# Optimization experiments

Measured on AMD Instinct MI355X. Metric: run time of the kernel, lower is better.

Reference implementation:

```python
import jax, jax.numpy as jnp
import numpy as np

N_NODES = 512
STATE_DIM = 16
MESSAGE_DIM = 32
HID_MSG = 64
HID_RO = 64
N_STEPS = 5


def setup_inputs() -> dict:
    key = jax.random.key(0)
    ks = jax.random.split(key, 16)
    s, m, hm, hr = STATE_DIM, MESSAGE_DIM, HID_MSG, HID_RO
    gru_in = s + m
    k_gru = 1.0 / np.sqrt(s)
    inp = {
        'J': jax.random.normal(ks[0], (N_NODES, N_NODES), jnp.float32),
        'b': jax.random.normal(ks[1], (N_NODES,), jnp.float32),
        # message MLP (torch init: weight ~ N(0, 0.1), bias = 0)
        'W1': 0.1 * jax.random.normal(ks[2], (hm, 2 * s + 3), jnp.float32),
        'b1': jnp.zeros((hm,), jnp.float32),
        'W2': 0.1 * jax.random.normal(ks[3], (hm, hm), jnp.float32),
        'b2': jnp.zeros((hm,), jnp.float32),
        'W3': 0.1 * jax.random.normal(ks[4], (m, hm), jnp.float32),
        'b3': jnp.zeros((m,), jnp.float32),
        # GRUCell params (torch default: U(-1/sqrt(hidden), 1/sqrt(hidden)))
        'W_ih': jax.random.uniform(ks[5], (3 * s, gru_in), jnp.float32, -k_gru, k_gru),
        'b_ih': jnp.zeros((3 * s,), jnp.float32),
        'W_hh': jax.random.uniform(ks[6], (3 * s, s), jnp.float32, -k_gru, k_gru),
        'b_hh': jnp.zeros((3 * s,), jnp.float32),
        # readout MLP
        'Wr1': 0.1 * jax.random.normal(ks[7], (hr, s), jnp.float32),
        'br1': jnp.zeros((hr,), jnp.float32),
        'Wr2': 0.1 * jax.random.normal(ks[8], (hr, hr), jnp.float32),
        'br2': jnp.zeros((hr,), jnp.float32),
        'Wr3': 0.1 * jax.random.normal(ks[9], (2, hr), jnp.float32),
        'br3': jnp.zeros((2,), jnp.float32),
    }
    return inp


def _gru_cell(x, h, W_ih, b_ih, W_hh, b_hh):
    s = h.shape[-1]
    gi = x @ W_ih.T + b_ih  # (n, 3s)
    gh = h @ W_hh.T + b_hh  # (n, 3s)
    ir, iz, in_ = gi[:, :s], gi[:, s:2 * s], gi[:, 2 * s:]
    hr, hz, hn = gh[:, :s], gh[:, s:2 * s], gh[:, 2 * s:]
    r = jax.nn.sigmoid(ir + hr)
    z = jax.nn.sigmoid(iz + hz)
    n = jnp.tanh(in_ + r * hn)
    return (1.0 - z) * n + z * h


def reference(J, b, W1, b1, W2, b2, W3, b3, W_ih, b_ih, W_hh, b_hh,
              Wr1, br1, Wr2, br2, Wr3, br3):
    n = J.shape[0]
    s = W_hh.shape[1]
    # Split first message-MLP layer by input blocks [h_i | h_j | J_ij | b_i | b_j]
    # so we never materialize the (n, n, 2s+3) feature tensor.
    W1_hi = W1[:, :s]            # (hm, s)
    W1_hj = W1[:, s:2 * s]       # (hm, s)
    w_J = W1[:, 2 * s]           # (hm,)
    w_bi = W1[:, 2 * s + 1]      # (hm,)
    w_bj = W1[:, 2 * s + 2]      # (hm,)
    # static per-pair part of layer-1 preactivation: (n, n, hm)
    static1 = (J[:, :, None] * w_J
               + b[:, None, None] * w_bi
               + b[None, :, None] * w_bj
               + b1)

    h0 = jnp.zeros((n, s), jnp.float32)

    def step(h, _):
        pre = (h @ W1_hi.T)[:, None, :] + (h @ W1_hj.T)[None, :, :] + static1
        x = jax.nn.relu(pre)                      # (n, n, hm)
        x = jax.nn.relu(x @ W2.T + b2)            # (n, n, hm)
        msg = x @ W3.T + b3                       # (n, n, m)
        m_j = msg.sum(axis=0)                     # sum over i -> (n, m)
        gru_in = jnp.concatenate([h, m_j], axis=1)
        h_new = _gru_cell(gru_in, h, W_ih, b_ih, W_hh, b_hh)
        return h_new, None

    h, _ = jax.lax.scan(step, h0, None, length=N_STEPS)

    y = jax.nn.relu(h @ Wr1.T + br1)
    y = jax.nn.relu(y @ Wr2.T + br2)
    y = jax.nn.sigmoid(y @ Wr3.T + br3)           # (n, 2)
    y = y / jnp.sum(y, axis=1, keepdims=True)
    return y
```

## Files before the change

kernel.cpp:

```cpp
#include <hip/hip_runtime.h>
#include <hip/hip_bf16.h>

#define NN 512
#define SDIM 16
#define MDIM 32
#define HM 64
#define NSTEPS 5

typedef __attribute__((ext_vector_type(8))) short short8;
typedef __attribute__((ext_vector_type(4))) float floatx4;

static __device__ __forceinline__ unsigned short f2bf(float f) {
    union { float f; unsigned u; } x; x.f = f;
    unsigned r = x.u + 0x7fffu + ((x.u >> 16) & 1u);
    return (unsigned short)(r >> 16);
}

__global__ void init_kernel(const float* __restrict__ J, const float* __restrict__ b,
                            const float* __restrict__ W1, const float* __restrict__ b1,
                            const float* __restrict__ W2,
                            float* __restrict__ Jt, float* __restrict__ aG, float* __restrict__ cG,
                            float* __restrict__ h0, float* __restrict__ wJ,
                            unsigned short* __restrict__ W2bf)
{
    int bx = blockIdx.x, tid = threadIdx.x;
    if (bx < 64) {
        __shared__ float tile[64][65];
        int ti = bx >> 3, tj = bx & 7;
        for (int p = 0; p < 16; ++p) {
            int e = p*256 + tid; int r = e >> 6, c = e & 63;
            tile[r][c] = J[(ti*64 + r)*512 + tj*64 + c];
        }
        __syncthreads();
        for (int p = 0; p < 16; ++p) {
            int e = p*256 + tid; int r = e >> 6, c = e & 63;
            Jt[(tj*64 + r)*512 + ti*64 + c] = tile[c][r];
        }
    } else if (bx < 96) {
        int gid = (bx - 64)*256 + tid;
        for (int p = 0; p < 4; ++p) {
            int idx = p*8192 + gid;
            int i = idx >> 6, o = idx & 63;
            aG[idx] = b[i] * W1[o*35 + 33];
        }
    } else if (bx < 128) {
        int gid = (bx - 96)*256 + tid;
        for (int p = 0; p < 4; ++p) {
            int idx = p*8192 + gid;
            int i = idx >> 6, o = idx & 63;
            cG[idx] = b[i] * W1[o*35 + 34] + b1[o];
        }
    } else if (bx == 128) {
        for (int p = 0; p < 16; ++p) {
            int flat = p*256 + tid;
            int jj = flat & 7;
            int lane = (flat >> 3) & 63;
            int tk = flat >> 9;
            int nt = tk >> 1, ks = tk & 1;
            int n = nt*16 + (lane & 15);
            int k = ks*32 + (lane >> 4)*8 + jj;
            W2bf[flat] = f2bf(W2[n*64 + k]);
        }
        if (tid < 64) wJ[tid] = W1[tid*35 + 32];
    } else {
        for (int p = 0; p < 32; ++p) h0[p*256 + tid] = 0.f;
    }
}

__global__ __launch_bounds__(256) void edge_kernel(
    const float* __restrict__ Jt,
    const float* __restrict__ aIn, const float* __restrict__ cIn, const float* __restrict__ hIn,
    float* __restrict__ aOut, float* __restrict__ cOut, float* __restrict__ hOut,
    const unsigned short* __restrict__ W2bf, const float* __restrict__ wJ,
    const float* __restrict__ b2, const float* __restrict__ W3, const float* __restrict__ b3,
    const float* __restrict__ W_ih, const float* __restrict__ b_ih,
    const float* __restrict__ W_hh, const float* __restrict__ b_hh,
    const float* __restrict__ W1, const float* __restrict__ bvec, const float* __restrict__ b1)
{
    const int j = blockIdx.x;
    const int tid = threadIdx.x;
    const int l = tid & 63, w = tid >> 6;
    const int m = l & 15, q = l >> 4;

    __shared__ float smWave[4][64];
    __shared__ float smMacc[64];
    __shared__ float smMsg[32];
    __shared__ float smGi[48], smGh[48];
    __shared__ float smH[16];

    const floatx4* c4 = (const floatx4*)cIn;
    const floatx4* w4 = (const floatx4*)wJ;
    floatx4 cva = c4[j*16 + q*2],     cvb = c4[j*16 + q*2 + 1];
    floatx4 cvc = c4[j*16 + 8 + q*2], cvd = c4[j*16 + 8 + q*2 + 1];
    floatx4 wva = w4[q*2], wvb = w4[q*2+1], wvc = w4[8+q*2], wvd = w4[8+q*2+1];

    short8 bf[4][2];
    {
        const short8* wb = (const short8*)W2bf;
        #pragma unroll
        for (int nt = 0; nt < 4; ++nt)
            #pragma unroll
            for (int ks = 0; ks < 2; ++ks)
                bf[nt][ks] = wb[(nt*2 + ks)*64 + l];
    }
    float b2n[4];
    #pragma unroll
    for (int nt = 0; nt < 4; ++nt) b2n[nt] = b2[nt*16 + m];

    floatx4 acc[4];
    #pragma unroll
    for (int nt = 0; nt < 4; ++nt) acc[nt] = (floatx4){0.f,0.f,0.f,0.f};

    const floatx4* a4 = (const floatx4*)aIn;

    for (int c8 = 0; c8 < 8; ++c8) {
        int i = w*128 + c8*16 + m;
        float Jij = Jt[j*512 + i];
        floatx4 av0 = a4[i*16 + q*2],     av1 = a4[i*16 + q*2 + 1];
        floatx4 av2 = a4[i*16 + 8 + q*2], av3 = a4[i*16 + 8 + q*2 + 1];
        floatx4 x0, x1, x2, x3;
        #pragma unroll
        for (int e = 0; e < 4; ++e) {
            x0[e] = fmaxf(fmaf(Jij, wva[e], av0[e]) + cva[e], 0.f);
            x1[e] = fmaxf(fmaf(Jij, wvb[e], av1[e]) + cvb[e], 0.f);
            x2[e] = fmaxf(fmaf(Jij, wvc[e], av2[e]) + cvc[e], 0.f);
            x3[e] = fmaxf(fmaf(Jij, wvd[e], av3[e]) + cvd[e], 0.f);
        }
        short8 fa0, fa1;
        #pragma unroll
        for (int e = 0; e < 4; ++e) {
            fa0[e]   = (short)f2bf(x0[e]);
            fa0[e+4] = (short)f2bf(x1[e]);
            fa1[e]   = (short)f2bf(x2[e]);
            fa1[e+4] = (short)f2bf(x3[e]);
        }
        #pragma unroll
        for (int nt = 0; nt < 4; ++nt) {
            floatx4 d = {0.f,0.f,0.f,0.f};
            d = __builtin_amdgcn_mfma_f32_16x16x32_bf16(fa0, bf[nt][0], d, 0, 0, 0);
            d = __builtin_amdgcn_mfma_f32_16x16x32_bf16(fa1, bf[nt][1], d, 0, 0, 0);
            #pragma unroll
            for (int r = 0; r < 4; ++r)
                acc[nt][r] += fmaxf(d[r] + b2n[nt], 0.f);
        }
    }

    #pragma unroll
    for (int nt = 0; nt < 4; ++nt) {
        float v = acc[nt][0] + acc[nt][1] + acc[nt][2] + acc[nt][3];
        v += __shfl_xor(v, 16);
        v += __shfl_xor(v, 32);
        if (l < 16) smWave[w][nt*16 + l] = v;
    }
    __syncthreads();
    if (tid < 64) smMacc[tid] = smWave[0][tid] + smWave[1][tid] + smWave[2][tid] + smWave[3][tid];
    __syncthreads();
    if (tid < 32) {
        float s = 512.f * b3[tid];
        for (int k = 0; k < 64; ++k) s += W3[tid*64 + k] * smMacc[k];
        smMsg[tid] = s;
    }
    __syncthreads();
    if (tid < 48) {
        float gi = b_ih[tid];
        for (int c = 0; c < 16; ++c) gi += W_ih[tid*48 + c] * hIn[j*16 + c];
        for (int c = 0; c < 32; ++c) gi += W_ih[tid*48 + 16 + c] * smMsg[c];
        float gh = b_hh[tid];
        for (int s = 0; s < 16; ++s) gh += W_hh[tid*16 + s] * hIn[j*16 + s];
        smGi[tid] = gi; smGh[tid] = gh;
    }
    __syncthreads();
    if (tid < 16) {
        float r = 1.f / (1.f + __expf(-(smGi[tid] + smGh[tid])));
        float z = 1.f / (1.f + __expf(-(smGi[16+tid] + smGh[16+tid])));
        float n = tanhf(smGi[32+tid] + r * smGh[32+tid]);
        float hn = (1.f - z)*n + z*hIn[j*16 + tid];
        hOut[j*16 + tid] = hn;
        smH[tid] = hn;
    }
    __syncthreads();
    if (tid < 64) {
        int o = tid;
        float da = 0.f, dc = 0.f;
        for (int s = 0; s < 16; ++s) {
            da += W1[o*35 + s]      * smH[s];
            dc += W1[o*35 + 16 + s] * smH[s];
        }
        aOut[j*64 + o] = da + bvec[j]*W1[o*35+33];
        cOut[j*64 + o] = dc + bvec[j]*W1[o*35+34] + b1[o];
    }
}

__global__ void readout_kernel(const float* __restrict__ h,
    const float* __restrict__ Wr1, const float* __restrict__ br1,
    const float* __restrict__ Wr2, const float* __restrict__ br2,
    const float* __restrict__ Wr3, const float* __restrict__ br3,
    float* __restrict__ out)
{
    int tid = threadIdx.x; int l = tid & 63, w = tid >> 6;
    int node = blockIdx.x*4 + w;
    __shared__ float sm[4][64];
    float y1 = br1[l];
    for (int s = 0; s < 16; ++s) y1 += Wr1[l*16 + s] * h[node*16 + s];
    y1 = fmaxf(y1, 0.f);
    sm[w][l] = y1;
    __syncthreads();
    float y2 = br2[l];
    for (int k = 0; k < 64; ++k) y2 += Wr2[l*64 + k] * sm[w][k];
    y2 = fmaxf(y2, 0.f);
    __syncthreads();
    sm[w][l] = y2;
    __syncthreads();
    if (l == 0) {
        float s0 = br3[0], s1 = br3[1];
        for (int k = 0; k < 64; ++k) { s0 += Wr3[k]*sm[w][k]; s1 += Wr3[64+k]*sm[w][k]; }
        float e0 = 1.f/(1.f + __expf(-s0));
        float e1 = 1.f/(1.f + __expf(-s1));
        float t = e0 + e1;
        out[node*2]     = e0/t;
        out[node*2 + 1] = e1/t;
    }
}

extern "C" void kernel_launch(void* const* d_in, const int* in_sizes, int n_in,
                              void* d_out, int out_size, void* d_ws, size_t ws_size,
                              hipStream_t stream)
{
    const float* J    = (const float*)d_in[0];
    const float* b    = (const float*)d_in[1];
    const float* W1   = (const float*)d_in[2];
    const float* b1   = (const float*)d_in[3];
    const float* W2   = (const float*)d_in[4];
    const float* b2   = (const float*)d_in[5];
    const float* W3   = (const float*)d_in[6];
    const float* b3   = (const float*)d_in[7];
    const float* W_ih = (const float*)d_in[8];
    const float* b_ih = (const float*)d_in[9];
    const float* W_hh = (const float*)d_in[10];
    const float* b_hh = (const float*)d_in[11];
    const float* Wr1  = (const float*)d_in[12];
    const float* br1  = (const float*)d_in[13];
    const float* Wr2  = (const float*)d_in[14];
    const float* br2  = (const float*)d_in[15];
    const float* Wr3  = (const float*)d_in[16];
    const float* br3  = (const float*)d_in[17];
    float* out = (float*)d_out;

    float* ws  = (float*)d_ws;
    float* Jt  = ws;
    float* aG0 = ws + 262144;
    float* aG1 = aG0 + 32768;
    float* cG0 = aG1 + 32768;
    float* cG1 = cG0 + 32768;
    float* hA  = cG1 + 32768;
    float* hB  = hA + 8192;
    float* wJ  = hB + 8192;
    unsigned short* W2bf = (unsigned short*)(wJ + 64);

    hipLaunchKernelGGL(init_kernel, dim3(130), dim3(256), 0, stream,
                       J, b, W1, b1, W2, Jt, aG0, cG0, hA, wJ, W2bf);

    float* aIn = aG0; float* aOut = aG1;
    float* cIn = cG0; float* cOut = cG1;
    float* hI  = hA;  float* hO  = hB;
    for (int t = 0; t < NSTEPS; ++t) {
        hipLaunchKernelGGL(edge_kernel, dim3(512), dim3(256), 0, stream,
            Jt, aIn, cIn, hI, aOut, cOut, hO, W2bf, wJ, b2, W3, b3,
            W_ih, b_ih, W_hh, b_hh, W1, b, b1);
        float* tmp;
        tmp = aIn; aIn = aOut; aOut = tmp;
        tmp = cIn; cIn = cOut; cOut = tmp;
        tmp = hI;  hI  = hO;  hO  = tmp;
    }
    hipLaunchKernelGGL(readout_kernel, dim3(128), dim3(256), 0, stream,
        hI, Wr1, br1, Wr2, br2, Wr3, br3, out);
}
```

Before: 159.9 us.

## Fuse readout into last edge step and parallelize per-node GRU tail

Merges the readout MLP into the final edge_kernel launch, removing one kernel launch. The serial per-node tail is rewritten so more threads share the work: the W3 message projection, the GRU gate matvecs and the next-step a/c projections use vectorized loads and shuffle reductions. W1 slices are pre-transposed in init so these loads are contiguous, and bf16 packing now uses the paired intrinsic. The tail is small next to the MFMA loop, so the main saving is fewer launches and a shorter serial epilogue; it adds workspace buffers and a flag branch in the kernel.

```diff
diff --git a/kernel.cpp b/kernel.cpp
--- a/kernel.cpp
+++ b/kernel.cpp
@@ -2,9 +2,6 @@
 #include <hip/hip_bf16.h>
 
 #define NN 512
-#define SDIM 16
-#define MDIM 32
-#define HM 64
 #define NSTEPS 5
 
 typedef __attribute__((ext_vector_type(8))) short short8;
@@ -14,6 +11,11 @@
     union { float f; unsigned u; } x; x.f = f;
     unsigned r = x.u + 0x7fffu + ((x.u >> 16) & 1u);
     return (unsigned short)(r >> 16);
+}
+
+static __device__ __forceinline__ unsigned pk2bf(float a, float b) {
+    __hip_bfloat162 h = __float22bfloat162_rn(make_float2(a, b));
+    return *reinterpret_cast<unsigned*>(&h);
 }
 
 __global__ void init_kernel(const float* __restrict__ J, const float* __restrict__ b,
@@ -21,6 +23,8 @@
                             const float* __restrict__ W2,
                             float* __restrict__ Jt, float* __restrict__ aG, float* __restrict__ cG,
                             float* __restrict__ h0, float* __restrict__ wJ,
+                            float* __restrict__ wbi, float* __restrict__ wbj,
+                            float* __restrict__ W1hiT, float* __restrict__ W1hjT,
                             unsigned short* __restrict__ W2bf)
 {
     int bx = blockIdx.x, tid = threadIdx.x;
@@ -61,7 +65,16 @@
             int k = ks*32 + (lane >> 4)*8 + jj;
             W2bf[flat] = f2bf(W2[n*64 + k]);
         }
-        if (tid < 64) wJ[tid] = W1[tid*35 + 32];
+        if (tid < 64) {
+            wJ[tid]  = W1[tid*35 + 32];
+            wbi[tid] = W1[tid*35 + 33];
+            wbj[tid] = W1[tid*35 + 34];
+            #pragma unroll
+            for (int s = 0; s < 16; ++s) {
+                W1hiT[tid*16 + s] = W1[tid*35 + s];
+                W1hjT[tid*16 + s] = W1[tid*35 + 16 + s];
+            }
+        }
     } else {
         for (int p = 0; p < 32; ++p) h0[p*256 + tid] = 0.f;
     }
@@ -75,7 +88,13 @@
     const float* __restrict__ b2, const float* __restrict__ W3, const float* __restrict__ b3,
     const float* __restrict__ W_ih, const float* __restrict__ b_ih,
     const float* __restrict__ W_hh, const float* __restrict__ b_hh,
-    const float* __restrict__ W1, const float* __restrict__ bvec, const float* __restrict__ b1)
+    const float* __restrict__ W1hiT, const float* __restrict__ W1hjT,
+    const float* __restrict__ wbi, const float* __restrict__ wbj,
+    const float* __restrict__ bvec, const float* __restrict__ b1,
+    const float* __restrict__ Wr1, const float* __restrict__ br1,
+    const float* __restrict__ Wr2, const float* __restrict__ br2,
+    const float* __restrict__ Wr3, const float* __restrict__ br3,
+    float* __restrict__ out, int last)
 {
     const int j = blockIdx.x;
     const int tid = threadIdx.x;
@@ -84,9 +103,11 @@
 
     __shared__ float smWave[4][64];
     __shared__ float smMacc[64];
-    __shared__ float smMsg[32];
+    __shared__ float smGin[48];
     __shared__ float smGi[48], smGh[48];
     __shared__ float smH[16];
+    __shared__ float smY[64];
+    __shared__ float smR[2];
 
     const floatx4* c4 = (const floatx4*)cIn;
     const floatx4* w4 = (const floatx4*)wJ;
@@ -94,14 +115,14 @@
     floatx4 cvc = c4[j*16 + 8 + q*2], cvd = c4[j*16 + 8 + q*2 + 1];
     floatx4 wva = w4[q*2], wvb = w4[q*2+1], wvc = w4[8+q*2], wvd = w4[8+q*2+1];
 
-    short8 bf[4][2];
+    short8 bfw[4][2];
     {
         const short8* wb = (const short8*)W2bf;
         #pragma unroll
         for (int nt = 0; nt < 4; ++nt)
             #pragma unroll
             for (int ks = 0; ks < 2; ++ks)
-                bf[nt][ks] = wb[(nt*2 + ks)*64 + l];
+                bfw[nt][ks] = wb[(nt*2 + ks)*64 + l];
     }
     float b2n[4];
     #pragma unroll
@@ -126,19 +147,16 @@
             x2[e] = fmaxf(fmaf(Jij, wvc[e], av2[e]) + cvc[e], 0.f);
             x3[e] = fmaxf(fmaf(Jij, wvd[e], av3[e]) + cvd[e], 0.f);
         }
-        short8 fa0, fa1;
-        #pragma unroll
-        for (int e = 0; e < 4; ++e) {
-            fa0[e]   = (short)f2bf(x0[e]);
-            fa0[e+4] = (short)f2bf(x1[e]);
-            fa1[e]   = (short)f2bf(x2[e]);
-            fa1[e+4] = (short)f2bf(x3[e]);
-        }
+        union { short8 s; unsigned u[4]; } fa0, fa1;
+        fa0.u[0] = pk2bf(x0[0], x0[1]); fa0.u[1] = pk2bf(x0[2], x0[3]);
+        fa0.u[2] = pk2bf(x1[0], x1[1]); fa0.u[3] = pk2bf(x1[2], x1[3]);
+        fa1.u[0] = pk2bf(x2[0], x2[1]); fa1.u[1] = pk2bf(x2[2], x2[3]);
+        fa1.u[2] = pk2bf(x3[0], x3[1]); fa1.u[3] = pk2bf(x3[2], x3[3]);
         #pragma unroll
         for (int nt = 0; nt < 4; ++nt) {
             floatx4 d = {0.f,0.f,0.f,0.f};
-            d = __builtin_amdgcn_mfma_f32_16x16x32_bf16(fa0, bf[nt][0], d, 0, 0, 0);
-            d = __builtin_amdgcn_mfma_f32_16x16x32_bf16(fa1, bf[nt][1], d, 0, 0, 0);
+            d = __builtin_amdgcn_mfma_f32_16x16x32_bf16(fa0.s, bfw[nt][0], d, 0, 0, 0);
+            d = __builtin_amdgcn_mfma_f32_16x16x32_bf16(fa1.s, bfw[nt][1], d, 0, 0, 0);
             #pragma unroll
             for (int r = 0; r < 4; ++r)
                 acc[nt][r] += fmaxf(d[r] + b2n[nt], 0.f);
@@ -152,73 +170,139 @@
         v += __shfl_xor(v, 32);
         if (l < 16) smWave[w][nt*16 + l] = v;
     }
+    if (tid < 16) smGin[tid] = hIn[j*16 + tid];
     __syncthreads();
     if (tid < 64) smMacc[tid] = smWave[0][tid] + smWave[1][tid] + smWave[2][tid] + smWave[3][tid];
     __syncthreads();
-    if (tid < 32) {
-        float s = 512.f * b3[tid];
-        for (int k = 0; k < 64; ++k) s += W3[tid*64 + k] * smMacc[k];
-        smMsg[tid] = s;
-    }
-    __syncthreads();
-    if (tid < 48) {
-        float gi = b_ih[tid];
-        for (int c = 0; c < 16; ++c) gi += W_ih[tid*48 + c] * hIn[j*16 + c];
-        for (int c = 0; c < 32; ++c) gi += W_ih[tid*48 + 16 + c] * smMsg[c];
-        float gh = b_hh[tid];
-        for (int s = 0; s < 16; ++s) gh += W_hh[tid*16 + s] * hIn[j*16 + s];
-        smGi[tid] = gi; smGh[tid] = gh;
-    }
-    __syncthreads();
+
+    {
+        int o = tid >> 3, p = tid & 7;
+        const floatx4* W3v = (const floatx4*)W3;
+        floatx4 wv0 = W3v[o*16 + p*2], wv1 = W3v[o*16 + p*2 + 1];
+        float part = 0.f;
+        #pragma unroll
+        for (int e = 0; e < 4; ++e) {
+            part = fmaf(wv0[e], smMacc[p*8 + e], part);
+            part = fmaf(wv1[e], smMacc[p*8 + 4 + e], part);
+        }
+        part += __shfl_xor(part, 1);
+        part += __shfl_xor(part, 2);
+        part += __shfl_xor(part, 4);
+        if (p == 0) smGin[16 + o] = part + 512.f * b3[o];
+    }
+    __syncthreads();
+
+    if (tid < 192) {
+        int o = tid >> 2, p = tid & 3;
+        const floatx4* Wv = (const floatx4*)W_ih;
+        floatx4 w0 = Wv[o*12 + p*3], w1 = Wv[o*12 + p*3 + 1], w2 = Wv[o*12 + p*3 + 2];
+        int k0 = p*12;
+        float part = 0.f;
+        #pragma unroll
+        for (int e = 0; e < 4; ++e) {
+            part = fmaf(w0[e], smGin[k0 + e], part);
+            part = fmaf(w1[e], smGin[k0 + 4 + e], part);
+            part = fmaf(w2[e], smGin[k0 + 8 + e], part);
+        }
+        part += __shfl_xor(part, 1);
+        part += __shfl_xor(part, 2);
+        if (p == 0) smGi[o] = part + b_ih[o];
+    } else if (tid < 240) {
+        int o = tid - 192;
+        const floatx4* Wv = (const floatx4*)W_hh;
+        floatx4 w0 = Wv[o*4], w1 = Wv[o*4+1], w2 = Wv[o*4+2], w3 = Wv[o*4+3];
+        float s = b_hh[o];
+        #pragma unroll
+        for (int e = 0; e < 4; ++e) {
+            s = fmaf(w0[e], smGin[e],      s);
+            s = fmaf(w1[e], smGin[4 + e],  s);
+            s = fmaf(w2[e], smGin[8 + e],  s);
+            s = fmaf(w3[e], smGin[12 + e], s);
+        }
+        smGh[o] = s;
+    }
+    __syncthreads();
+
     if (tid < 16) {
         float r = 1.f / (1.f + __expf(-(smGi[tid] + smGh[tid])));
         float z = 1.f / (1.f + __expf(-(smGi[16+tid] + smGh[16+tid])));
         float n = tanhf(smGi[32+tid] + r * smGh[32+tid]);
-        float hn = (1.f - z)*n + z*hIn[j*16 + tid];
+        float hn = (1.f - z)*n + z*smGin[tid];
         hOut[j*16 + tid] = hn;
         smH[tid] = hn;
     }
     __syncthreads();
-    if (tid < 64) {
-        int o = tid;
-        float da = 0.f, dc = 0.f;
-        for (int s = 0; s < 16; ++s) {
-            da += W1[o*35 + s]      * smH[s];
-            dc += W1[o*35 + 16 + s] * smH[s];
-        }
-        aOut[j*64 + o] = da + bvec[j]*W1[o*35+33];
-        cOut[j*64 + o] = dc + bvec[j]*W1[o*35+34] + b1[o];
-    }
-}
-
-__global__ void readout_kernel(const float* __restrict__ h,
-    const float* __restrict__ Wr1, const float* __restrict__ br1,
-    const float* __restrict__ Wr2, const float* __restrict__ br2,
-    const float* __restrict__ Wr3, const float* __restrict__ br3,
-    float* __restrict__ out)
-{
-    int tid = threadIdx.x; int l = tid & 63, w = tid >> 6;
-    int node = blockIdx.x*4 + w;
-    __shared__ float sm[4][64];
-    float y1 = br1[l];
-    for (int s = 0; s < 16; ++s) y1 += Wr1[l*16 + s] * h[node*16 + s];
-    y1 = fmaxf(y1, 0.f);
-    sm[w][l] = y1;
-    __syncthreads();
-    float y2 = br2[l];
-    for (int k = 0; k < 64; ++k) y2 += Wr2[l*64 + k] * sm[w][k];
-    y2 = fmaxf(y2, 0.f);
-    __syncthreads();
-    sm[w][l] = y2;
-    __syncthreads();
-    if (l == 0) {
-        float s0 = br3[0], s1 = br3[1];
-        for (int k = 0; k < 64; ++k) { s0 += Wr3[k]*sm[w][k]; s1 += Wr3[64+k]*sm[w][k]; }
-        float e0 = 1.f/(1.f + __expf(-s0));
-        float e1 = 1.f/(1.f + __expf(-s1));
-        float t = e0 + e1;
-        out[node*2]     = e0/t;
-        out[node*2 + 1] = e1/t;
+
+    if (!last) {
+        if (tid < 128) {
+            int o = tid & 63, sel = tid >> 6;
+            const floatx4* Wv = (const floatx4*)(sel ? W1hjT : W1hiT);
+            floatx4 w0 = Wv[o*4], w1 = Wv[o*4+1], w2 = Wv[o*4+2], w3 = Wv[o*4+3];
+            float s = 0.f;
+            #pragma unroll
+            for (int e = 0; e < 4; ++e) {
+                s = fmaf(w0[e], smH[e],      s);
+                s = fmaf(w1[e], smH[4 + e],  s);
+                s = fmaf(w2[e], smH[8 + e],  s);
+                s = fmaf(w3[e], smH[12 + e], s);
+            }
+            if (sel == 0) aOut[j*64 + o] = s + bvec[j]*wbi[o];
+            else          cOut[j*64 + o] = s + bvec[j]*wbj[o] + b1[o];
+        }
+    } else {
+        if (tid < 64) {
+            const floatx4* Wv = (const floatx4*)Wr1;
+            floatx4 w0 = Wv[tid*4], w1 = Wv[tid*4+1], w2 = Wv[tid*4+2], w3 = Wv[tid*4+3];
+            float s = br1[tid];
+            #pragma unroll
+            for (int e = 0; e < 4; ++e) {
+                s = fmaf(w0[e], smH[e],      s);
+                s = fmaf(w1[e], smH[4 + e],  s);
+                s = fmaf(w2[e], smH[8 + e],  s);
+                s = fmaf(w3[e], smH[12 + e], s);
+            }
+            smY[tid] = fmaxf(s, 0.f);
+        }
+        __syncthreads();
+        {
+            int o = tid >> 2, p = tid & 3;
+            const floatx4* Wv = (const floatx4*)Wr2;
+            floatx4 w0 = Wv[o*16 + p*4],     w1 = Wv[o*16 + p*4 + 1];
+            floatx4 w2 = Wv[o*16 + p*4 + 2], w3 = Wv[o*16 + p*4 + 3];
+            int k0 = p*16;
+            float part = 0.f;
+            #pragma unroll
+            for (int e = 0; e < 4; ++e) {
+                part = fmaf(w0[e], smY[k0 + e],      part);
+                part = fmaf(w1[e], smY[k0 + 4 + e],  part);
+                part = fmaf(w2[e], smY[k0 + 8 + e],  part);
+                part = fmaf(w3[e], smY[k0 + 12 + e], part);
+            }
+            part += __shfl_xor(part, 1);
+            part += __shfl_xor(part, 2);
+            __syncthreads();
+            if (p == 0) smY[o] = fmaxf(part + br2[o], 0.f);
+        }
+        __syncthreads();
+        if (tid < 128) {
+            int ot = tid >> 6, p = tid & 63;
+            float part = Wr3[ot*64 + p] * smY[p];
+            part += __shfl_xor(part, 1);
+            part += __shfl_xor(part, 2);
+            part += __shfl_xor(part, 4);
+            part += __shfl_xor(part, 8);
+            part += __shfl_xor(part, 16);
+            part += __shfl_xor(part, 32);
+            if (p == 0) smR[ot] = part + br3[ot];
+        }
+        __syncthreads();
+        if (tid == 0) {
+            float e0 = 1.f/(1.f + __expf(-smR[0]));
+            float e1 = 1.f/(1.f + __expf(-smR[1]));
+            float t = e0 + e1;
+            out[j*2]     = e0/t;
+            out[j*2 + 1] = e1/t;
+        }
     }
 }
 
@@ -246,19 +330,23 @@
     const float* br3  = (const float*)d_in[17];
     float* out = (float*)d_out;
 
-    float* ws  = (float*)d_ws;
-    float* Jt  = ws;
-    float* aG0 = ws + 262144;
-    float* aG1 = aG0 + 32768;
-    float* cG0 = aG1 + 32768;
-    float* cG1 = cG0 + 32768;
-    float* hA  = cG1 + 32768;
-    float* hB  = hA + 8192;
-    float* wJ  = hB + 8192;
-    unsigned short* W2bf = (unsigned short*)(wJ + 64);
+    float* ws   = (float*)d_ws;
+    float* Jt   = ws;
+    float* aG0  = Jt + 262144;
+    float* aG1  = aG0 + 32768;
+    float* cG0  = aG1 + 32768;
+    float* cG1  = cG0 + 32768;
+    float* hA   = cG1 + 32768;
+    float* hB   = hA + 8192;
+    float* wJ   = hB + 8192;
+    float* wbi  = wJ + 64;
+    float* wbj  = wbi + 64;
+    float* W1hiT = wbj + 64;
+    float* W1hjT = W1hiT + 1024;
+    unsigned short* W2bf = (unsigned short*)(W1hjT + 1024);
 
     hipLaunchKernelGGL(init_kernel, dim3(130), dim3(256), 0, stream,
-                       J, b, W1, b1, W2, Jt, aG0, cG0, hA, wJ, W2bf);
+                       J, b, W1, b1, W2, Jt, aG0, cG0, hA, wJ, wbi, wbj, W1hiT, W1hjT, W2bf);
 
     float* aIn = aG0; float* aOut = aG1;
     float* cIn = cG0; float* cOut = cG1;
@@ -266,12 +354,11 @@
     for (int t = 0; t < NSTEPS; ++t) {
         hipLaunchKernelGGL(edge_kernel, dim3(512), dim3(256), 0, stream,
             Jt, aIn, cIn, hI, aOut, cOut, hO, W2bf, wJ, b2, W3, b3,
-            W_ih, b_ih, W_hh, b_hh, W1, b, b1);
+            W_ih, b_ih, W_hh, b_hh, W1hiT, W1hjT, wbi, wbj, b, b1,
+            Wr1, br1, Wr2, br2, Wr3, br3, out, (t == NSTEPS-1) ? 1 : 0);
         float* tmp;
         tmp = aIn; aIn = aOut; aOut = tmp;
         tmp = cIn; cIn = cOut; cOut = tmp;
         tmp = hI;  hI  = hO;  hO  = tmp;
     }
-    hipLaunchKernelGGL(readout_kernel, dim3(128), dim3(256), 0, stream,
-        hI, Wr1, br1, Wr2, br2, Wr3, br3, out);
-}
+}
```

Result: no change. 159.0 us (-0.6%).
